# Performance work log

Hardware: AMD Instinct MI355X
Metric: run time of the kernel (lower is better)

The kernel has to match this reference:

```python
import jax, jax.numpy as jnp
import numpy as np

# Config (matches init_kwargs): complex RG-LRU, sigmoid gates, gate_a_imag='same',
# fixed input norm, log_a_scale=-8.0
B, S, D_IN = 4, 4096, 1024
D_HID = 2048            # merged (real|imag) hidden width
D_INNER = D_HID // 2    # complex channels
NB = 8                  # n_diag_blocks
LOG_A_SCALE = -8.0
R_MIN, R_MAX = 0.9, 0.999


def _bdl(x, w, b):
    """BlockDiagonalLinear: x (B,S,d_in) -> (B,S,nb*bout). w: (nb,bin,bout), b: (nb*bout,)."""
    Bb, Ss, d = x.shape
    nb, bin_, bout = w.shape
    xb = x.reshape(Bb, Ss, nb, bin_)
    y = jnp.einsum('bsni,nio->bsno', xb, w) + b.reshape(nb, bout)
    return y.reshape(Bb, Ss, nb * bout)


def setup_inputs() -> dict:
    key = jax.random.key(0)
    ks = jax.random.split(key, 10)
    x = jax.random.normal(ks[0], (B, S, D_IN), dtype=jnp.float32)
    # input Dense(d_hidden)
    w_in = jax.random.normal(ks[1], (D_IN, D_HID), dtype=jnp.float32) / np.sqrt(D_IN)
    b_in = jnp.zeros((D_HID,), jnp.float32)
    # BlockDiagonalLinear weights for gate_x and gate_a
    bin_, bout = D_HID // NB, D_INNER // NB
    w_gx = jax.random.normal(ks[2], (NB, bin_, bout), dtype=jnp.float32) / np.sqrt(bin_)
    b_gx = jnp.zeros((D_INNER,), jnp.float32)
    w_ga = jax.random.normal(ks[3], (NB, bin_, bout), dtype=jnp.float32) / np.sqrt(bin_)
    b_ga = jnp.zeros((D_INNER,), jnp.float32)
    # stable_init_real: softplus(param) = -0.5*log(u*(rmax^2-rmin^2)+rmin^2)
    u = jax.random.uniform(ks[4], (D_INNER,))
    a_real = 0.5 * jnp.log(u * (R_MAX**2 - R_MIN**2) + R_MIN**2 + 1e-8)
    a_real_param = jnp.log(jnp.exp(-a_real) - 1.0)
    # stable_init_imag: pi * init_maxval_imag * u, init_maxval_imag = 0.1
    a_imag_param = jnp.pi * 0.1 * jax.random.uniform(ks[5], (D_INNER,))
    # output Dense(d_in)
    w_out = jax.random.normal(ks[6], (D_HID, D_IN), dtype=jnp.float32) / np.sqrt(D_HID)
    b_out = jnp.zeros((D_IN,), jnp.float32)
    return dict(x=x, w_in=w_in, b_in=b_in, w_gx=w_gx, b_gx=b_gx, w_ga=w_ga,
                b_ga=b_ga, a_real_param=a_real_param, a_imag_param=a_imag_param,
                w_out=w_out, b_out=b_out)


def reference(x, w_in, b_in, w_gx, b_gx, w_ga, b_ga, a_real_param, a_imag_param,
              w_out, b_out):
    xh = x @ w_in + b_in                                  # (B,S,D_HID)
    gate_x = jax.nn.sigmoid(_bdl(xh, w_gx, b_gx))         # (B,S,D_INNER)
    gate_a = jax.nn.sigmoid(_bdl(xh, w_ga, b_ga))         # (B,S,D_INNER)
    # log_a = scale * gate_a_real * softplus(a_real_param)  (negative => |a|<1)
    log_a = LOG_A_SCALE * gate_a * jax.nn.softplus(a_real_param)
    log_a_imag = a_imag_param * gate_a                    # gate_a_imag = 'same'
    a = jnp.exp(jax.lax.complex(log_a, log_a_imag))       # complex decay (B,S,D_INNER)
    # merged_to_complex: first half real, second half imag
    xc = jax.lax.complex(xh[..., :D_INNER], xh[..., D_INNER:])
    xc = gate_x * xc
    # fixed input norm: sqrt(1 - |a|^2) = sqrt(1 - exp(2*log_a))
    norm = jnp.sqrt(jnp.maximum(1.0 - jnp.exp(2.0 * log_a), 1e-6))
    xc = norm * xc
    # linear recurrence h_t = a_t*h_{t-1} + x_t via parallel associative scan
    def combine(l, r):
        return (r[0] * l[0], r[0] * l[1] + r[1])
    _, h = jax.lax.associative_scan(combine, (a, xc), axis=1)  # h0 = 0
    h_m = jnp.concatenate([h.real, h.imag], axis=-1)      # complex_to_merged (B,S,D_HID)
    y = h_m @ w_out + b_out                               # (B,S,D_IN)
    h_last = h_m[:, -1]                                   # (B,D_HID)
    return y, h_last
```

## Files before the change

kernel.cpp:

```cpp
#include <hip/hip_runtime.h>
#include <cstdint>
#include <cstddef>

typedef short bf16x8 __attribute__((ext_vector_type(8)));
typedef float f32x4 __attribute__((ext_vector_type(4)));

__device__ __forceinline__ float b2f(ushort u) {
    union { float f; uint32_t i; } v; v.i = ((uint32_t)u) << 16; return v.f;
}
__device__ __forceinline__ ushort f2b(float f) {
    union { float f; uint32_t i; } v; v.f = f;
    uint32_t r = v.i + 0x7FFFu + ((v.i >> 16) & 1u);
    return (ushort)(r >> 16);
}

#define ASYNC16(g, l) \
    __builtin_amdgcn_global_load_lds((const __attribute__((address_space(1))) void*)(g), \
                                     (__attribute__((address_space(3))) void*)(l), 16, 0, 0)

__global__ void cvt_x_kernel(const float4* __restrict__ x, ushort4* __restrict__ xb) {
    int i = blockIdx.x * 256 + threadIdx.x;
    float4 v = x[i];
    ushort4 o; o.x = f2b(v.x); o.y = f2b(v.y); o.z = f2b(v.z); o.w = f2b(v.w);
    xb[i] = o;
}

__global__ void prep_w_kernel(const float* __restrict__ w_in, const float* __restrict__ w_out,
                              const float* __restrict__ w_gx, const float* __restrict__ w_ga,
                              const float* __restrict__ b_gx, const float* __restrict__ b_ga,
                              const float* __restrict__ arp,
                              ushort* __restrict__ w_inT, ushort* __restrict__ w_outT,
                              ushort* __restrict__ WgT, float* __restrict__ bg,
                              float* __restrict__ sp) {
    int idx = blockIdx.x * 256 + threadIdx.x;
    { int n = idx >> 10, k = idx & 1023; w_inT[idx]  = f2b(w_in[(size_t)k * 2048 + n]); }
    { int n = idx >> 11, k = idx & 2047; w_outT[idx] = f2b(w_out[(size_t)k * 1024 + n]); }
    if (idx < 524288) {
        int cv = idx >> 8, k = idx & 255;
        int nb = cv >> 8, r = cv & 255;
        float v = (r < 128) ? w_gx[(size_t)nb * 32768 + (size_t)k * 128 + r]
                            : w_ga[(size_t)nb * 32768 + (size_t)k * 128 + (r - 128)];
        WgT[idx] = f2b(v);
    }
    if (idx < 2048) {
        int nb = idx >> 8, r = idx & 255;
        bg[idx] = (r < 128) ? b_gx[nb * 128 + r] : b_ga[nb * 128 + r - 128];
    }
    if (idx < 1024) {
        sp[idx] = log1pf(__expf(arp[idx]));
    }
}

template<int EPI>
__launch_bounds__(256, 2)
__global__ void gemm_bt(const ushort* __restrict__ A, const ushort* __restrict__ B,
                        int M, int N, int K, int lda, int ldb,
                        const float* __restrict__ bias,
                        float* __restrict__ o0,
                        ushort* __restrict__ ob, ushort* __restrict__ ob1) {
    __shared__ ushort At[128 * 32];
    __shared__ ushort Bt[128 * 32];
    const int tid = threadIdx.x;
    const int lane = tid & 63;
    const int wave = tid >> 6;
    const int wr = wave >> 1, wc = wave & 1;
    const int m0 = blockIdx.y * 128, n0 = blockIdx.x * 128;

    const ushort* Ab = A;
    if (EPI == 1) Ab += (size_t)(n0 >> 8) * 256;

    const int arow = tid >> 2;
    const int acolb = (tid & 3) << 4;
    const char* ag0 = (const char*)Ab + ((size_t)(m0 + arow) * lda) * 2 + acolb;
    const char* ag1 = ag0 + (size_t)64 * lda * 2;
    const char* bg0 = (const char*)B + ((size_t)(n0 + arow) * ldb) * 2 + acolb;
    const char* bg1 = bg0 + (size_t)64 * ldb * 2;
    ushort* la0 = At + tid * 8; ushort* la1 = la0 + 2048;
    ushort* lb0 = Bt + tid * 8; ushort* lb1 = lb0 + 2048;

    f32x4 acc[4][4];
#pragma unroll
    for (int i = 0; i < 4; ++i)
#pragma unroll
        for (int j = 0; j < 4; ++j) acc[i][j] = (f32x4){0.f, 0.f, 0.f, 0.f};

    const int fm = lane & 15;
    const int fko = (lane >> 4) * 8;
    const ushort* Af = At + (wr * 64 + fm) * 32 + fko;
    const ushort* Bf = Bt + (wc * 64 + fm) * 32 + fko;

    const int nk = K >> 5;
    for (int kk = 0; kk < nk; ++kk) {
        __syncthreads();
        const size_t off = (size_t)kk * 64;
        ASYNC16(ag0 + off, la0);
        ASYNC16(ag1 + off, la1);
        ASYNC16(bg0 + off, lb0);
        ASYNC16(bg1 + off, lb1);
        __syncthreads();
        bf16x8 af[4], bfv[4];
#pragma unroll
        for (int i = 0; i < 4; ++i) af[i]  = *(const bf16x8*)(Af + i * 512);
#pragma unroll
        for (int i = 0; i < 4; ++i) bfv[i] = *(const bf16x8*)(Bf + i * 512);
#pragma unroll
        for (int i = 0; i < 4; ++i)
#pragma unroll
            for (int j = 0; j < 4; ++j)
                acc[i][j] = __builtin_amdgcn_mfma_f32_16x16x32_bf16(af[i], bfv[j], acc[i][j], 0, 0, 0);
    }

    const int r0 = (lane >> 4) * 4;
    const int cn = lane & 15;
#pragma unroll
    for (int j = 0; j < 4; ++j) {
        const int n = n0 + wc * 64 + j * 16 + cn;
        const float bv = bias[n];
        if (EPI == 1) {
            const int nb = n >> 8, rr = n & 255;
            const int c = nb * 128 + (rr & 127);
            ushort* base = (rr < 128) ? ob : ob1;
#pragma unroll
            for (int i = 0; i < 4; ++i) {
                const int mb = m0 + wr * 64 + i * 16 + r0;
#pragma unroll
                for (int r = 0; r < 4; ++r) {
                    float v = acc[i][j][r] + bv;
                    base[(size_t)(mb + r) * 1024 + c] = f2b(1.f / (1.f + __expf(-v)));
                }
            }
        } else if (EPI == 0) {
#pragma unroll
            for (int i = 0; i < 4; ++i) {
                const int mb = m0 + wr * 64 + i * 16 + r0;
#pragma unroll
                for (int r = 0; r < 4; ++r)
                    ob[(size_t)(mb + r) * N + n] = f2b(acc[i][j][r] + bv);
            }
        } else {
#pragma unroll
            for (int i = 0; i < 4; ++i) {
                const int mb = m0 + wr * 64 + i * 16 + r0;
#pragma unroll
                for (int r = 0; r < 4; ++r)
                    o0[(size_t)(mb + r) * N + n] = acc[i][j][r] + bv;
            }
        }
    }
}

template<int FINAL>
__global__ void scan_chunk(const ushort* __restrict__ gx, const ushort* __restrict__ ga,
                           ushort* __restrict__ xhb,
                           const float* __restrict__ sp, const float* __restrict__ aim,
                           float2* __restrict__ carryA, float2* __restrict__ carryH,
                           const float2* __restrict__ prefixH,
                           float* __restrict__ hlast) {
    const int c = blockIdx.y * 256 + threadIdx.x;
    const int b = blockIdx.z;
    const int chunk = blockIdx.x;
    const int m0 = b * 4096 + chunk * 64;
    const float spc = sp[c], amc = aim[c];
    float Ar = 1.f, Ai = 0.f, Hr = 0.f, Hi = 0.f;
    if (FINAL) { float2 p = prefixH[chunk * 4096 + b * 1024 + c]; Hr = p.x; Hi = p.y; }
#pragma unroll 4
    for (int t = 0; t < 64; ++t) {
        const size_t m = (size_t)(m0 + t);
        float gxv = b2f(gx[m * 1024 + c]);
        float gav = b2f(ga[m * 1024 + c]);
        float xr = b2f(xhb[m * 2048 + c]);
        float xi = b2f(xhb[m * 2048 + c + 1024]);
        float la = -8.f * gav * spc;
        float er = __expf(la);
        float th = amc * gav;
        float sn, cs; __sincosf(th, &sn, &cs);
        float ar = er * cs, ai = er * sn;
        float nr = sqrtf(fmaxf(1.f - er * er, 1e-6f));
        float f = nr * gxv;
        float xcr = f * xr, xci = f * xi;
        float h2 = ar * Hr - ai * Hi + xcr;
        Hi = ar * Hi + ai * Hr + xci; Hr = h2;
        if (FINAL) {
            xhb[m * 2048 + c] = f2b(Hr);
            xhb[m * 2048 + c + 1024] = f2b(Hi);
        } else {
            float a2 = ar * Ar - ai * Ai; Ai = ar * Ai + ai * Ar; Ar = a2;
        }
    }
    if (!FINAL) {
        int s = chunk * 4096 + b * 1024 + c;
        carryA[s] = make_float2(Ar, Ai);
        carryH[s] = make_float2(Hr, Hi);
    } else if (chunk == 63) {
        hlast[b * 2048 + c] = Hr;
        hlast[b * 2048 + c + 1024] = Hi;
    }
}

__global__ void scan_top(const float2* __restrict__ cA, const float2* __restrict__ cH,
                         float2* __restrict__ pH) {
    const int s = blockIdx.x * 256 + threadIdx.x;
    float pr = 0.f, pi = 0.f;
    for (int ch = 0; ch < 64; ++ch) {
        pH[ch * 4096 + s] = make_float2(pr, pi);
        float2 A = cA[ch * 4096 + s];
        float2 H = cH[ch * 4096 + s];
        float t = A.x * pr - A.y * pi + H.x;
        pi = A.x * pi + A.y * pr + H.y;
        pr = t;
    }
}

__global__ void ws_report_kernel(float* out, float code) {
    out[blockIdx.x * 256 + threadIdx.x] = code;
}

extern "C" void kernel_launch(void* const* d_in, const int* in_sizes, int n_in,
                              void* d_out, int out_size, void* d_ws, size_t ws_size,
                              hipStream_t stream) {
    const float* x     = (const float*)d_in[0];
    const float* w_in  = (const float*)d_in[1];
    const float* b_in  = (const float*)d_in[2];
    const float* w_gx  = (const float*)d_in[3];
    const float* b_gx  = (const float*)d_in[4];
    const float* w_ga  = (const float*)d_in[5];
    const float* b_ga  = (const float*)d_in[6];
    const float* arp   = (const float*)d_in[7];
    const float* aip   = (const float*)d_in[8];
    const float* w_out = (const float*)d_in[9];
    const float* b_out = (const float*)d_in[10];
    float* out = (float*)d_out;

    char* p = (char*)d_ws;
    ushort* R0    = (ushort*)p; p += 67108864;
    ushort* xb    = R0;
    ushort* gxb   = R0;
    ushort* gab   = R0 + 16777216;
    ushort* xhb   = (ushort*)p; p += 67108864;
    ushort* w_inT = (ushort*)p; p += 4194304;
    ushort* w_outT= (ushort*)p; p += 4194304;
    ushort* WgT   = (ushort*)p; p += 1048576;
    float*  bg    = (float*)p;  p += 8192;
    float*  sp    = (float*)p;  p += 4096;
    float2* cA    = (float2*)p; p += 2097152;
    float2* cH    = (float2*)p; p += 2097152;
    float2* pH    = (float2*)p; p += 2097152;
    size_t need = (size_t)(p - (char*)d_ws);
    if (ws_size < need) {
        float code = 1000.0f + (float)(ws_size >> 20);
        ws_report_kernel<<<64, 256, 0, stream>>>(out, code);
        return;
    }

    cvt_x_kernel<<<16384, 256, 0, stream>>>((const float4*)x, (ushort4*)xb);
    prep_w_kernel<<<8192, 256, 0, stream>>>(w_in, w_out, w_gx, w_ga, b_gx, b_ga, arp,
                                            w_inT, w_outT, WgT, bg, sp);
    gemm_bt<0><<<dim3(16, 128), 256, 0, stream>>>(xb, w_inT, 16384, 2048, 1024, 1024, 1024,
                                                  b_in, nullptr, xhb, nullptr);
    gemm_bt<1><<<dim3(16, 128), 256, 0, stream>>>(xhb, WgT, 16384, 2048, 256, 2048, 256,
                                                  bg, nullptr, gxb, gab);
    scan_chunk<0><<<dim3(64, 4, 4), 256, 0, stream>>>(gxb, gab, xhb, sp, aip, cA, cH,
                                                      nullptr, nullptr);
    scan_top<<<16, 256, 0, stream>>>(cA, cH, pH);
    scan_chunk<1><<<dim3(64, 4, 4), 256, 0, stream>>>(gxb, gab, xhb, sp, aip, nullptr, nullptr,
                                                      pH, out + 16777216);
    gemm_bt<2><<<dim3(8, 128), 256, 0, stream>>>(xhb, w_outT, 16384, 1024, 2048, 2048, 2048,
                                                 b_out, out, nullptr, nullptr);
}
```

Before: 448.4 us.

## Tile weight transposes, swizzle GEMM block order, vectorize scan over channel pairs

Replaces the strided per-element weight transpose/convert with LDS-tiled transposes that read float4 and write 8-wide bf16, plus a tiny kernel for biases and softplus. GEMMs now use a 1D grid with a block-index swizzle, meant to improve L2 reuse of A/B tiles across concurrently running blocks. The scan kernels process two adjacent channels per thread with ushort2 loads and stores, halving the thread count but doubling the memory access width. It adds four extra small launches and lowers scan parallelism in exchange.

```diff
diff --git a/kernel.cpp b/kernel.cpp
--- a/kernel.cpp
+++ b/kernel.cpp
@@ -3,6 +3,7 @@
 #include <cstddef>
 
 typedef short bf16x8 __attribute__((ext_vector_type(8)));
+typedef ushort ushort8 __attribute__((ext_vector_type(8)));
 typedef float f32x4 __attribute__((ext_vector_type(4)));
 
 __device__ __forceinline__ float b2f(ushort u) {
@@ -25,36 +26,54 @@
     xb[i] = o;
 }
 
-__global__ void prep_w_kernel(const float* __restrict__ w_in, const float* __restrict__ w_out,
-                              const float* __restrict__ w_gx, const float* __restrict__ w_ga,
-                              const float* __restrict__ b_gx, const float* __restrict__ b_ga,
-                              const float* __restrict__ arp,
-                              ushort* __restrict__ w_inT, ushort* __restrict__ w_outT,
-                              ushort* __restrict__ WgT, float* __restrict__ bg,
-                              float* __restrict__ sp) {
+__global__ void transpose_cvt(const float* __restrict__ in, ushort* __restrict__ out,
+                              int R, int C, int outStride,
+                              size_t inBatch, size_t outBatch) {
+    __shared__ float t[64 * 65];
+    const int tid = threadIdx.x;
+    const int r0 = blockIdx.y * 64, c0 = blockIdx.x * 64;
+    const float* inp = in + blockIdx.z * inBatch;
+    ushort* outp = out + blockIdx.z * outBatch;
+
+    const int lr = tid >> 4;
+    const int lc = (tid & 15) * 4;
+#pragma unroll
+    for (int i = 0; i < 4; ++i) {
+        const int row = lr + i * 16;
+        const float4 v = *(const float4*)&inp[(size_t)(r0 + row) * C + c0 + lc];
+        t[row * 65 + lc + 0] = v.x;
+        t[row * 65 + lc + 1] = v.y;
+        t[row * 65 + lc + 2] = v.z;
+        t[row * 65 + lc + 3] = v.w;
+    }
+    __syncthreads();
+    const int oc = tid >> 2;
+    const int orr = (tid & 3) * 16;
+    ushort8 a, b;
+#pragma unroll
+    for (int i = 0; i < 8; ++i) a[i] = f2b(t[(orr + i) * 65 + oc]);
+#pragma unroll
+    for (int i = 0; i < 8; ++i) b[i] = f2b(t[(orr + 8 + i) * 65 + oc]);
+    ushort* dst = outp + (size_t)(c0 + oc) * outStride + r0 + orr;
+    *(ushort8*)dst = a;
+    *(ushort8*)(dst + 8) = b;
+}
+
+__global__ void prep_small_kernel(const float* __restrict__ b_gx, const float* __restrict__ b_ga,
+                                  const float* __restrict__ arp,
+                                  float* __restrict__ bg, float* __restrict__ sp) {
     int idx = blockIdx.x * 256 + threadIdx.x;
-    { int n = idx >> 10, k = idx & 1023; w_inT[idx]  = f2b(w_in[(size_t)k * 2048 + n]); }
-    { int n = idx >> 11, k = idx & 2047; w_outT[idx] = f2b(w_out[(size_t)k * 1024 + n]); }
-    if (idx < 524288) {
-        int cv = idx >> 8, k = idx & 255;
-        int nb = cv >> 8, r = cv & 255;
-        float v = (r < 128) ? w_gx[(size_t)nb * 32768 + (size_t)k * 128 + r]
-                            : w_ga[(size_t)nb * 32768 + (size_t)k * 128 + (r - 128)];
-        WgT[idx] = f2b(v);
-    }
-    if (idx < 2048) {
+    {
         int nb = idx >> 8, r = idx & 255;
         bg[idx] = (r < 128) ? b_gx[nb * 128 + r] : b_ga[nb * 128 + r - 128];
     }
-    if (idx < 1024) {
-        sp[idx] = log1pf(__expf(arp[idx]));
-    }
+    if (idx < 1024) sp[idx] = log1pf(__expf(arp[idx]));
 }
 
 template<int EPI>
 __launch_bounds__(256, 2)
 __global__ void gemm_bt(const ushort* __restrict__ A, const ushort* __restrict__ B,
-                        int M, int N, int K, int lda, int ldb,
+                        int M, int N, int K, int lda, int ldb, int gxbits,
                         const float* __restrict__ bias,
                         float* __restrict__ o0,
                         ushort* __restrict__ ob, ushort* __restrict__ ob1) {
@@ -64,7 +83,10 @@
     const int lane = tid & 63;
     const int wave = tid >> 6;
     const int wr = wave >> 1, wc = wave & 1;
-    const int m0 = blockIdx.y * 128, n0 = blockIdx.x * 128;
+
+    const int swz = (blockIdx.x & 7) * (gridDim.x >> 3) + (blockIdx.x >> 3);
+    const int m0 = (swz >> gxbits) * 128;
+    const int n0 = (swz & ((1 << gxbits) - 1)) * 128;
 
     const ushort* Ab = A;
     if (EPI == 1) Ab += (size_t)(n0 >> 8) * 256;
@@ -73,8 +95,8 @@
     const int acolb = (tid & 3) << 4;
     const char* ag0 = (const char*)Ab + ((size_t)(m0 + arow) * lda) * 2 + acolb;
     const char* ag1 = ag0 + (size_t)64 * lda * 2;
-    const char* bg0 = (const char*)B + ((size_t)(n0 + arow) * ldb) * 2 + acolb;
-    const char* bg1 = bg0 + (size_t)64 * ldb * 2;
+    const char* bgp0 = (const char*)B + ((size_t)(n0 + arow) * ldb) * 2 + acolb;
+    const char* bgp1 = bgp0 + (size_t)64 * ldb * 2;
     ushort* la0 = At + tid * 8; ushort* la1 = la0 + 2048;
     ushort* lb0 = Bt + tid * 8; ushort* lb1 = lb0 + 2048;
 
@@ -95,8 +117,8 @@
         const size_t off = (size_t)kk * 64;
         ASYNC16(ag0 + off, la0);
         ASYNC16(ag1 + off, la1);
-        ASYNC16(bg0 + off, lb0);
-        ASYNC16(bg1 + off, lb1);
+        ASYNC16(bgp0 + off, lb0);
+        ASYNC16(bgp1 + off, lb1);
         __syncthreads();
         bf16x8 af[4], bfv[4];
 #pragma unroll
@@ -150,50 +172,73 @@
 }
 
 template<int FINAL>
-__global__ void scan_chunk(const ushort* __restrict__ gx, const ushort* __restrict__ ga,
-                           ushort* __restrict__ xhb,
+__global__ void scan_chunk(const ushort2* __restrict__ gx2, const ushort2* __restrict__ ga2,
+                           ushort2* __restrict__ xhb2,
                            const float* __restrict__ sp, const float* __restrict__ aim,
                            float2* __restrict__ carryA, float2* __restrict__ carryH,
                            const float2* __restrict__ prefixH,
                            float* __restrict__ hlast) {
-    const int c = blockIdx.y * 256 + threadIdx.x;
+    const int c2 = blockIdx.y * 256 + threadIdx.x;
+    const int c = c2 * 2;
     const int b = blockIdx.z;
     const int chunk = blockIdx.x;
     const int m0 = b * 4096 + chunk * 64;
-    const float spc = sp[c], amc = aim[c];
-    float Ar = 1.f, Ai = 0.f, Hr = 0.f, Hi = 0.f;
-    if (FINAL) { float2 p = prefixH[chunk * 4096 + b * 1024 + c]; Hr = p.x; Hi = p.y; }
+    const float sp0 = sp[c], sp1 = sp[c + 1];
+    const float am0 = aim[c], am1 = aim[c + 1];
+    float Ar0 = 1.f, Ai0 = 0.f, Hr0 = 0.f, Hi0 = 0.f;
+    float Ar1 = 1.f, Ai1 = 0.f, Hr1 = 0.f, Hi1 = 0.f;
+    if (FINAL) {
+        float2 p0 = prefixH[chunk * 4096 + b * 1024 + c];
+        float2 p1 = prefixH[chunk * 4096 + b * 1024 + c + 1];
+        Hr0 = p0.x; Hi0 = p0.y; Hr1 = p1.x; Hi1 = p1.y;
+    }
 #pragma unroll 4
     for (int t = 0; t < 64; ++t) {
         const size_t m = (size_t)(m0 + t);
-        float gxv = b2f(gx[m * 1024 + c]);
-        float gav = b2f(ga[m * 1024 + c]);
-        float xr = b2f(xhb[m * 2048 + c]);
-        float xi = b2f(xhb[m * 2048 + c + 1024]);
-        float la = -8.f * gav * spc;
-        float er = __expf(la);
-        float th = amc * gav;
-        float sn, cs; __sincosf(th, &sn, &cs);
-        float ar = er * cs, ai = er * sn;
-        float nr = sqrtf(fmaxf(1.f - er * er, 1e-6f));
-        float f = nr * gxv;
-        float xcr = f * xr, xci = f * xi;
-        float h2 = ar * Hr - ai * Hi + xcr;
-        Hi = ar * Hi + ai * Hr + xci; Hr = h2;
+        const ushort2 gv = gx2[m * 512 + c2];
+        const ushort2 av = ga2[m * 512 + c2];
+        const ushort2 xrv = xhb2[m * 1024 + c2];
+        const ushort2 xiv = xhb2[m * 1024 + 512 + c2];
+        {
+            float gav = b2f(av.x);
+            float er = __expf(-8.f * gav * sp0);
+            float sn, cs; __sincosf(am0 * gav, &sn, &cs);
+            float f = sqrtf(fmaxf(1.f - er * er, 1e-6f)) * b2f(gv.x);
+            float ar = er * cs, ai = er * sn;
+            float xcr = f * b2f(xrv.x), xci = f * b2f(xiv.x);
+            float h2 = ar * Hr0 - ai * Hi0 + xcr;
+            Hi0 = ar * Hi0 + ai * Hr0 + xci; Hr0 = h2;
+            if (!FINAL) { float a2 = ar * Ar0 - ai * Ai0; Ai0 = ar * Ai0 + ai * Ar0; Ar0 = a2; }
+        }
+        {
+            float gav = b2f(av.y);
+            float er = __expf(-8.f * gav * sp1);
+            float sn, cs; __sincosf(am1 * gav, &sn, &cs);
+            float f = sqrtf(fmaxf(1.f - er * er, 1e-6f)) * b2f(gv.y);
+            float ar = er * cs, ai = er * sn;
+            float xcr = f * b2f(xrv.y), xci = f * b2f(xiv.y);
+            float h2 = ar * Hr1 - ai * Hi1 + xcr;
+            Hi1 = ar * Hi1 + ai * Hr1 + xci; Hr1 = h2;
+            if (!FINAL) { float a2 = ar * Ar1 - ai * Ai1; Ai1 = ar * Ai1 + ai * Ar1; Ar1 = a2; }
+        }
         if (FINAL) {
-            xhb[m * 2048 + c] = f2b(Hr);
-            xhb[m * 2048 + c + 1024] = f2b(Hi);
-        } else {
-            float a2 = ar * Ar - ai * Ai; Ai = ar * Ai + ai * Ar; Ar = a2;
+            ushort2 hr; hr.x = f2b(Hr0); hr.y = f2b(Hr1);
+            ushort2 hi; hi.x = f2b(Hi0); hi.y = f2b(Hi1);
+            xhb2[m * 1024 + c2] = hr;
+            xhb2[m * 1024 + 512 + c2] = hi;
         }
     }
     if (!FINAL) {
         int s = chunk * 4096 + b * 1024 + c;
-        carryA[s] = make_float2(Ar, Ai);
-        carryH[s] = make_float2(Hr, Hi);
+        carryA[s] = make_float2(Ar0, Ai0);
+        carryA[s + 1] = make_float2(Ar1, Ai1);
+        carryH[s] = make_float2(Hr0, Hi0);
+        carryH[s + 1] = make_float2(Hr1, Hi1);
     } else if (chunk == 63) {
-        hlast[b * 2048 + c] = Hr;
-        hlast[b * 2048 + c + 1024] = Hi;
+        hlast[b * 2048 + c] = Hr0;
+        hlast[b * 2048 + c + 1] = Hr1;
+        hlast[b * 2048 + c + 1024] = Hi0;
+        hlast[b * 2048 + c + 1025] = Hi1;
     }
 }
 
@@ -253,17 +298,23 @@
     }
 
     cvt_x_kernel<<<16384, 256, 0, stream>>>((const float4*)x, (ushort4*)xb);
-    prep_w_kernel<<<8192, 256, 0, stream>>>(w_in, w_out, w_gx, w_ga, b_gx, b_ga, arp,
-                                            w_inT, w_outT, WgT, bg, sp);
-    gemm_bt<0><<<dim3(16, 128), 256, 0, stream>>>(xb, w_inT, 16384, 2048, 1024, 1024, 1024,
-                                                  b_in, nullptr, xhb, nullptr);
-    gemm_bt<1><<<dim3(16, 128), 256, 0, stream>>>(xhb, WgT, 16384, 2048, 256, 2048, 256,
-                                                  bg, nullptr, gxb, gab);
-    scan_chunk<0><<<dim3(64, 4, 4), 256, 0, stream>>>(gxb, gab, xhb, sp, aip, cA, cH,
+    transpose_cvt<<<dim3(32, 16, 1), 256, 0, stream>>>(w_in, w_inT, 1024, 2048, 1024, 0, 0);
+    transpose_cvt<<<dim3(16, 32, 1), 256, 0, stream>>>(w_out, w_outT, 2048, 1024, 2048, 0, 0);
+    transpose_cvt<<<dim3(2, 4, 8), 256, 0, stream>>>(w_gx, WgT, 256, 128, 256, 32768, 65536);
+    transpose_cvt<<<dim3(2, 4, 8), 256, 0, stream>>>(w_ga, WgT + 32768, 256, 128, 256, 32768, 65536);
+    prep_small_kernel<<<8, 256, 0, stream>>>(b_gx, b_ga, arp, bg, sp);
+
+    gemm_bt<0><<<2048, 256, 0, stream>>>(xb, w_inT, 16384, 2048, 1024, 1024, 1024, 4,
+                                         b_in, nullptr, xhb, nullptr);
+    gemm_bt<1><<<2048, 256, 0, stream>>>(xhb, WgT, 16384, 2048, 256, 2048, 256, 4,
+                                         bg, nullptr, gxb, gab);
+    scan_chunk<0><<<dim3(64, 2, 4), 256, 0, stream>>>((const ushort2*)gxb, (const ushort2*)gab,
+                                                      (ushort2*)xhb, sp, aip, cA, cH,
                                                       nullptr, nullptr);
     scan_top<<<16, 256, 0, stream>>>(cA, cH, pH);
-    scan_chunk<1><<<dim3(64, 4, 4), 256, 0, stream>>>(gxb, gab, xhb, sp, aip, nullptr, nullptr,
+    scan_chunk<1><<<dim3(64, 2, 4), 256, 0, stream>>>((const ushort2*)gxb, (const ushort2*)gab,
+                                                      (ushort2*)xhb, sp, aip, nullptr, nullptr,
                                                       pH, out + 16777216);
-    gemm_bt<2><<<dim3(8, 128), 256, 0, stream>>>(xhb, w_outT, 16384, 1024, 2048, 2048, 2048,
-                                                 b_out, out, nullptr, nullptr);
-}
+    gemm_bt<2><<<1024, 256, 0, stream>>>(xhb, w_outT, 16384, 1024, 2048, 2048, 2048, 3,
+                                         b_out, out, nullptr, nullptr);
+}
```

Result: faster. 425.5 us (-5.1%).
